# Kernel tuning notes

Measured on AMD Instinct MI355X. Metric: run time of the kernel, lower is better.

## Reference

```python
import jax, jax.numpy as jnp
import numpy as np

B = 128
IN = 256
NLVL = 6
KLVL = 3
CH = 4
C = 4 * CH * CH          # 64 channels per node
OU = 8                   # out_filter_siz_u
OV = 8                   # out_filter_siz_v
NK = 2 ** KLVL           # 8 leaf nodes per axis
W_SCALE = 1.0 / 16.0     # ~1/sqrt(2*2*C) so 7 stacked relu-convs stay numerically sane


def setup_inputs() -> dict:
    key = jax.random.key(0)
    ks = jax.random.split(key, 2 * NLVL + 4)
    fx = IN // 2 ** NLVL  # 4: input patch filter size
    inp = {}
    inp["in_data"] = jax.random.normal(ks[0], (B, IN, IN, 1), jnp.float32)
    inp["in_filter"] = jax.random.normal(ks[1], (fx, fx, 1, C), jnp.float32) * W_SCALE
    inp["in_bias"] = jnp.zeros((C,), jnp.float32)
    i = 2
    for lvl in range(1, NLVL + 1):
        n = 2 ** min(lvl, KLVL)  # node grid: grows to 2^klvl then stays
        inp[f"f{lvl}"] = jax.random.normal(ks[i], (n, n, 2, 2, C, C), jnp.float32) * W_SCALE
        inp[f"b{lvl}"] = jnp.zeros((n, n, C), jnp.float32)
        i += 1
    inp["Wd"] = jax.random.normal(ks[i], (NK, NK, 2, C, OU * OV), jnp.float32) * W_SCALE
    return inp


def _node_conv(x, w, b):
    # x: [Nu,Nv,B,H,W,C]; w: [Nu,Nv,2,2,C,C]; 2x2 stride-2 VALID conv per node
    Nu, Nv, Bn, H, W, Cc = x.shape
    xr = x.reshape(Nu, Nv, Bn, H // 2, 2, W // 2, 2, Cc)
    y = jnp.einsum('uvbhxwyc,uvxyco->uvbhwo', xr, w)
    return jax.nn.relu(y + b[:, :, None, None, None, :])


def _forward(in_data, in_filter, in_bias, fs, bs, Wd):
    Bn = in_data.shape[0]
    fx, fy = in_filter.shape[0], in_filter.shape[1]
    # input interp conv: stride == kernel -> non-overlapping patch GEMM
    xr = in_data[..., 0].reshape(Bn, in_data.shape[1] // fx, fx, in_data.shape[2] // fy, fy)
    x = jax.nn.relu(jnp.einsum('bxpyq,pqc->bxyc', xr, in_filter[:, :, 0, :]) + in_bias)
    x = x[None, None]  # [1,1,B,2^nlvl,2^nlvl,C] node grid
    for lvl in range(1, NLVL + 1):
        if lvl <= KLVL:
            # children (itu,itv) read parent (itu//2, itv//2)
            x = jnp.repeat(jnp.repeat(x, 2, axis=0), 2, axis=1)
        x = _node_conv(x, fs[lvl - 1], bs[lvl - 1])
    feats = x[:, :, :, 0, 0, :]  # [NK,NK,B,C]; spatial is 1x1 at level nlvl
    out = jnp.einsum('uvbc,uvrck->uvbrk', feats, Wd)  # r in {real, imag}
    out = out.reshape(NK, NK, Bn, 2, OU, OV)
    out = jnp.transpose(out, (2, 0, 4, 1, 5, 3))  # [B,itu,ou,itv,ov,2]
    return out.reshape(Bn, NK * OU, NK * OV, 2)


def reference(in_data, in_filter, in_bias, f1, b1, f2, b2, f3, b3, f4, b4, f5, b5, f6, b6, Wd):
    fs = (f1, f2, f3, f4, f5, f6)
    bs = (b1, b2, b3, b4, b5, b6)
    return _forward(in_data, in_filter, in_bias, fs, bs, Wd)
```

## Files before the change

kernel.cpp:

```cpp
#include <hip/hip_runtime.h>
#include <hip/hip_bf16.h>
#include <cstdint>
#include <cstddef>


typedef __attribute__((ext_vector_type(8))) short short8;
typedef __attribute__((ext_vector_type(4))) float f32x4;
typedef unsigned short ushort_t;

static __device__ __forceinline__ float b2f(const __hip_bfloat16 x) {
    return __bfloat162float(x);
}
static __device__ __forceinline__ ushort_t f2bf(float x) {
    __hip_bfloat16 h = __float2bfloat16(x);
    ushort_t u;
    __builtin_memcpy(&u, &h, 2);
    return u;
}
static __device__ __forceinline__ void gl_lds16(const void* g, void* l) {
    __builtin_amdgcn_global_load_lds(
        (const __attribute__((address_space(1))) void*)g,
        (__attribute__((address_space(3))) void*)l, 16, 0, 0);
}
#define WAIT_LGKM0() __builtin_amdgcn_s_waitcnt(0xC07F)
#define WAIT_VM0()   __builtin_amdgcn_s_waitcnt(0x0F70)

#define PREP_BLOCKS 2533

static __device__ __forceinline__ void prep_work(
    int gid, int isbf,
    const void* f1, const void* f2, const void* f3,
    const void* f4, const void* f5, const void* f6, const void* wdsrc,
    const void* b1, const void* b2, const void* b3,
    const void* b4, const void* b5, const void* b6,
    ushort_t* __restrict__ wbuf, ushort_t* __restrict__ wdbuf,
    float* __restrict__ bbuf)
{
    if (gid >= 648448) return;
    if (gid >= 630784) {
        const int bg = gid - 630784;
        const void* src; int base;
        if      (bg <   256) { src = b1; base = 0;     }
        else if (bg <  1280) { src = b2; base = 256;   }
        else if (bg <  5376) { src = b3; base = 1280;  }
        else if (bg <  9472) { src = b4; base = 5376;  }
        else if (bg < 13568) { src = b5; base = 9472;  }
        else                 { src = b6; base = 13568; }
        const int local = bg - base;
        bbuf[bg] = isbf ? b2f(((const __hip_bfloat16*)src)[local])
                        : ((const float*)src)[local];
        return;
    }
    if (gid >= 565248) {
        const int local = gid - 565248;
        const int lane = local & 63;
        const int slot = (local >> 6) & 15;
        const int site = local >> 10;
        const int ks2 = slot >> 3, nh = slot & 7, q = lane >> 4;
        const int n = nh * 16 + (lane & 15);
        const int r = n >> 6, kk = n & 63;
        const int cbase = ks2 * 32 + q * 8;
        ushort_t pk[8];
        if (isbf) {
            const ushort_t* s = (const ushort_t*)wdsrc;
            #pragma unroll
            for (int j = 0; j < 8; j++)
                pk[j] = s[(((size_t)(site * 2 + r) * 64 + cbase + j) * 64) + kk];
        } else {
            const float* s = (const float*)wdsrc;
            #pragma unroll
            for (int j = 0; j < 8; j++)
                pk[j] = f2bf(s[(((size_t)(site * 2 + r) * 64 + cbase + j) * 64) + kk]);
        }
        *(uint4*)&wdbuf[(size_t)local * 8] = *(uint4*)pk;
        return;
    }
    const void* fsrc; int base;
    if      (gid <   8192) { fsrc = f1; base = 0;      }
    else if (gid <  40960) { fsrc = f2; base = 8192;   }
    else if (gid < 172032) { fsrc = f3; base = 40960;  }
    else if (gid < 303104) { fsrc = f4; base = 172032; }
    else if (gid < 434176) { fsrc = f5; base = 303104; }
    else                   { fsrc = f6; base = 434176; }
    const int local = gid - base;
    const int lane = local & 63;
    const int slot = (local >> 6) & 7;
    const int sitetap = local >> 9;
    const int ks = slot >> 2, nh = slot & 3, q = lane >> 4;
    const int n = (lane & 15) + nh * 16;
    const int kbase = ks * 32 + q * 8;
    ushort_t pk[8];
    if (isbf) {
        const ushort_t* s = (const ushort_t*)fsrc + (size_t)sitetap * 4096;
        #pragma unroll
        for (int j = 0; j < 8; j++) pk[j] = s[(kbase + j) * 64 + n];
    } else {
        const float* s = (const float*)fsrc + (size_t)sitetap * 4096;
        #pragma unroll
        for (int j = 0; j < 8; j++) pk[j] = f2bf(s[(kbase + j) * 64 + n]);
    }
    *(uint4*)&wbuf[(size_t)gid * 8] = *(uint4*)pk;
}

static __device__ __forceinline__ void stage0_body(
    int blk, int isbf,
    const void* __restrict__ in_data, const void* __restrict__ filt,
    const void* __restrict__ bias, __hip_bfloat16* __restrict__ x0,
    int b_off, int Bc)
{
    const int X  = blk & 63;
    const int bl = blk >> 6;
    const int bg = bl + b_off;

    __shared__ float sIn[4][256];
    __shared__ float sF[16][64];
    __shared__ float sB[64];

    const int t = threadIdx.x;
    const size_t srow = ((size_t)bg * 256 + (size_t)X * 4) * 256;

    if (isbf) {
        const __hip_bfloat16* src = (const __hip_bfloat16*)in_data + srow;
        #pragma unroll
        for (int i = 0; i < 4; i++) {
            int flat = i * 256 + t;
            int p = flat >> 8, col = flat & 255;
            sIn[p][col] = b2f(src[(size_t)p * 256 + col]);
        }
        const __hip_bfloat16* fsrc = (const __hip_bfloat16*)filt;
        #pragma unroll
        for (int i = 0; i < 4; i++) {
            int flat = i * 256 + t;
            sF[flat >> 6][flat & 63] = b2f(fsrc[flat]);
        }
        if (t < 64) sB[t] = b2f(((const __hip_bfloat16*)bias)[t]);
    } else {
        const float* src = (const float*)in_data + srow;
        const int p = t >> 6, c4 = (t & 63) * 4;
        *(float4*)&sIn[p][c4] = *(const float4*)(src + (size_t)p * 256 + c4);
        const float* fsrc = (const float*)filt;
        #pragma unroll
        for (int i = 0; i < 4; i++) {
            int flat = i * 256 + t;
            sF[flat >> 6][flat & 63] = fsrc[flat];
        }
        if (t < 64) sB[t] = ((const float*)bias)[t];
    }
    __syncthreads();

    const int ty = t >> 4;
    const int tc = t & 15;

    float acc[4][4];
    {
        const float4 bv = *(const float4*)&sB[tc * 4];
        #pragma unroll
        for (int yi = 0; yi < 4; yi++) {
            acc[yi][0] = bv.x; acc[yi][1] = bv.y;
            acc[yi][2] = bv.z; acc[yi][3] = bv.w;
        }
    }

    #pragma unroll
    for (int p = 0; p < 4; p++) {
        float4 rin[4], rf[4];
        #pragma unroll
        for (int yi = 0; yi < 4; yi++)
            rin[yi] = *(const float4*)&sIn[p][ty * 16 + yi * 4];
        #pragma unroll
        for (int q = 0; q < 4; q++)
            rf[q] = *(const float4*)&sF[p * 4 + q][tc * 4];
        #pragma unroll
        for (int yi = 0; yi < 4; yi++) {
            #pragma unroll
            for (int q = 0; q < 4; q++) {
                const float a = ((const float*)&rin[yi])[q];
                acc[yi][0] = fmaf(a, rf[q].x, acc[yi][0]);
                acc[yi][1] = fmaf(a, rf[q].y, acc[yi][1]);
                acc[yi][2] = fmaf(a, rf[q].z, acc[yi][2]);
                acc[yi][3] = fmaf(a, rf[q].w, acc[yi][3]);
            }
        }
    }

    ushort_t* dst = (ushort_t*)x0;
    #pragma unroll
    for (int yi = 0; yi < 4; yi++) {
        uint2 pk;
        pk.x = (uint32_t)f2bf(fmaxf(acc[yi][0], 0.f))
             | ((uint32_t)f2bf(fmaxf(acc[yi][1], 0.f)) << 16);
        pk.y = (uint32_t)f2bf(fmaxf(acc[yi][2], 0.f))
             | ((uint32_t)f2bf(fmaxf(acc[yi][3], 0.f)) << 16);
        const int wpos = ty * 4 + yi;
        *(uint2*)(dst + ((size_t)(X * 64 + wpos) * Bc + bl) * 64 + tc * 4) = pk;
    }
}

__global__ __launch_bounds__(256) void k_prep0(
    const void* __restrict__ in_data,
    const void* f1, const void* f2, const void* f3,
    const void* f4, const void* f5, const void* f6, const void* wdsrc,
    const void* b1, const void* b2, const void* b3,
    const void* b4, const void* b5, const void* b6,
    ushort_t* __restrict__ wbuf, ushort_t* __restrict__ wdbuf,
    float* __restrict__ bbuf, int* __restrict__ flag,
    const void* __restrict__ filt, const void* __restrict__ bias0,
    __hip_bfloat16* __restrict__ x0, int Bc)
{
    __shared__ int sflag;
    const int t = threadIdx.x;
    if (t < 64) {
        const float v = __uint_as_float(((const uint32_t*)in_data)[t]);
        const bool plaus = (v == 0.0f) || (fabsf(v) > 1e-8f && fabsf(v) < 1e4f);
        const unsigned long long m = __ballot(plaus);
        if (t == 0) sflag = (__popcll(m) >= 48) ? 0 : 1;
    }
    __syncthreads();
    const int isbf = sflag;

    if (blockIdx.x < PREP_BLOCKS) {
        if (blockIdx.x == 0 && t == 0) *flag = isbf;
        prep_work(blockIdx.x * 256 + t, isbf,
                  f1, f2, f3, f4, f5, f6, wdsrc,
                  b1, b2, b3, b4, b5, b6, wbuf, wdbuf, bbuf);
    } else {
        stage0_body(blockIdx.x - PREP_BLOCKS, isbf, in_data, filt, bias0, x0, 0, Bc);
    }
}

__global__ __launch_bounds__(256) void k_stage0(
    const void* __restrict__ in_data, const void* __restrict__ filt,
    const void* __restrict__ bias, __hip_bfloat16* __restrict__ x0,
    const int* __restrict__ flag, int b_off, int Bc)
{
    stage0_body(blockIdx.x, *flag, in_data, filt, bias, x0, b_off, Bc);
}

__global__ __launch_bounds__(256, 2) void k_fused12(
    const __hip_bfloat16* __restrict__ xin,
    const ushort_t* __restrict__ w1,
    const ushort_t* __restrict__ w2,
    const float* __restrict__ b1, const float* __restrict__ b2,
    __hip_bfloat16* __restrict__ xout,
    int Bc, int mtiles)
{
    __shared__ __align__(16) ushort_t smem[34816];

    int idx = blockIdx.x;
    const int mt = idx % mtiles; idx /= mtiles;
    const int parent = idx & 3; idx >>= 2;
    const int wstrip = idx & 3;
    const int h2p = idx >> 2;
    const int ip = parent >> 1, jp = parent & 1;

    const int t = threadIdx.x;
    const int wave = t >> 6, lane = t & 63;
    const int lm = lane & 15, lq = lane >> 4;

    const size_t pstride = (size_t)Bc * 64;

    int brow = mt * 16 + lm;
    if (brow >= Bc) brow = Bc - 1;

    const ushort_t* w1site = w1 + (size_t)parent * 16384 + lane * 8;
    short8 breg[32];
    #pragma unroll
    for (int s = 0; s < 32; s++) breg[s] = *(const short8*)(w1site + s * 512);
    __builtin_amdgcn_sched_barrier(0);

    float bv1[4];
    #pragma unroll
    for (int fn = 0; fn < 4; fn++) bv1[fn] = b1[parent * 64 + fn * 16 + lm];

    const f32x4 zero = {0.f, 0.f, 0.f, 0.f};
    ushort_t* l1b = smem + 16384;
    const int wa = wave >> 1, wb = wave & 1;

    for (int pos = 0; pos < 4; pos++) {
        const int w2p = wstrip * 4 + pos;
        __syncthreads();

        #pragma unroll
        for (int k = 0; k < 4; k++) {
            const int lpos = wave * 4 + k;
            const int i0 = lpos >> 2, j0 = lpos & 3;
            const size_t poff =
                ((size_t)(4 * h2p + i0) * 64 + (4 * w2p + j0)) * pstride;
            #pragma unroll
            for (int ks = 0; ks < 2; ks++) {
                gl_lds16(xin + poff + (size_t)brow * 64 + ks * 32 + lq * 8,
                         &smem[(lpos * 2 + ks) * 512]);
            }
        }
        __syncthreads();

        f32x4 acc[4];
        #pragma unroll
        for (int fn = 0; fn < 4; fn++) acc[fn] = zero;
        #pragma unroll
        for (int cd = 0; cd < 4; cd++) {
            const int lpos = (2 * wa + (cd >> 1)) * 4 + (2 * wb + (cd & 1));
            #pragma unroll
            for (int ks = 0; ks < 2; ks++) {
                short8 afr = *(const short8*)&smem[(lpos * 2 + ks) * 512 + lane * 8];
                #pragma unroll
                for (int fn = 0; fn < 4; fn++)
                    acc[fn] = __builtin_amdgcn_mfma_f32_16x16x32_bf16(
                        afr, breg[cd * 8 + ks * 4 + fn], acc[fn], 0, 0, 0);
            }
        }
        ushort_t* dst = l1b + (pos * 4 + wave) * 1152;
        #pragma unroll
        for (int fn = 0; fn < 4; fn++) {
            #pragma unroll
            for (int r = 0; r < 4; r++) {
                const int m = lq * 4 + r;
                dst[m * 72 + fn * 16 + lm] =
                    f2bf(fmaxf(acc[fn][r] + bv1[fn], 0.f));
            }
        }
    }
    __syncthreads();

    {
        const int di = wave >> 1, dj = wave & 1;
        const int s2 = (2 * ip + di) * 4 + (2 * jp + dj);
        const ushort_t* w2site = w2 + (size_t)s2 * 16384 + lane * 8;
        short8 wreg[32];
        #pragma unroll
        for (int s = 0; s < 32; s++) wreg[s] = *(const short8*)(w2site + s * 512);
        __builtin_amdgcn_sched_barrier(0);

        float bv2[4];
        #pragma unroll
        for (int fn = 0; fn < 4; fn++) bv2[fn] = b2[s2 * 64 + fn * 16 + lm];

        ushort_t* so_buf = smem + wave * 2176;

        for (int pos = 0; pos < 4; pos++) {
            const int w2p = wstrip * 4 + pos;
            f32x4 acc[4];
            #pragma unroll
            for (int fn = 0; fn < 4; fn++) acc[fn] = zero;

            #pragma unroll
            for (int ab = 0; ab < 4; ab++) {
                const ushort_t* sl = l1b + (pos * 4 + ab) * 1152;
                #pragma unroll
                for (int ks = 0; ks < 2; ks++) {
                    short8 afr = *(const short8*)&sl[lm * 72 + ks * 32 + lq * 8];
                    #pragma unroll
                    for (int fn = 0; fn < 4; fn++)
                        acc[fn] = __builtin_amdgcn_mfma_f32_16x16x32_bf16(
                            afr, wreg[ab * 8 + ks * 4 + fn], acc[fn], 0, 0, 0);
                }
            }

            #pragma unroll
            for (int fn = 0; fn < 4; fn++) {
                #pragma unroll
                for (int r = 0; r < 4; r++) {
                    const int m = lq * 4 + r;
                    so_buf[m * 68 + fn * 16 + lm] =
                        f2bf(fmaxf(acc[fn][r] + bv2[fn], 0.f));
                }
            }
            const size_t obase = ((size_t)s2 * 256 + h2p * 16 + w2p) * pstride;
            #pragma unroll
            for (int i2 = 0; i2 < 2; i2++) {
                const int task = i2 * 64 + lane;
                const int oct = task & 7, row = task >> 3;
                const int brw = mt * 16 + row;
                if (brw < Bc) {
                    *(uint4*)(xout + obase + (size_t)brw * 64 + oct * 8) =
                        *(const uint4*)&so_buf[row * 68 + oct * 8];
                }
            }
        }
    }
}

__global__ __launch_bounds__(256, 2) void k_level4(
    const __hip_bfloat16* __restrict__ xin,
    const ushort_t* __restrict__ wbuf,
    const float* __restrict__ bbuf,
    __hip_bfloat16* __restrict__ xout,
    int Nv_out, int HW, int Bc, int mtiles)
{
    __shared__ __align__(16) ushort_t smem[17408];

    int idx = blockIdx.x;
    const int mt = idx % mtiles; idx /= mtiles;
    const int w  = idx % HW; idx /= HW;
    const int h  = idx % HW; idx /= HW;
    const int Nv_in = Nv_out >> 1;
    const int vp = idx % Nv_in;
    const int up = idx / Nv_in;

    const int t = threadIdx.x;
    const int wave = t >> 6, lane = t & 63;
    const int lm = lane & 15, lq = lane >> 4;

    const int so = (2 * up + (wave >> 1)) * Nv_out + (2 * vp + (wave & 1));
    const int H_in = HW * 2;
    const size_t pstride = (size_t)Bc * 64;
    const size_t siteb = (size_t)(up * Nv_in + vp) * H_in * H_in * pstride;
    const ushort_t* wsite = wbuf + (size_t)so * 4 * 4096 + lane * 8;

    {
        const int hi = 2 * h + (wave >> 1), wi = 2 * w + (wave & 1);
        const size_t tapoff = siteb + ((size_t)hi * H_in + wi) * pstride;
        #pragma unroll
        for (int j = 0; j < 8; j++) {
            const int ks = j >> 2, mh = j & 3;
            int b = mt * 64 + mh * 16 + lm;
            if (b >= Bc) b = Bc - 1;
            gl_lds16(xin + tapoff + (size_t)b * 64 + ks * 32 + lq * 8,
                     &smem[(wave * 8 + j) * 512]);
        }
    }

    short8 breg[32];
    #pragma unroll
    for (int s = 0; s < 32; s++)
        breg[s] = *(const short8*)(wsite + s * 512);
    __builtin_amdgcn_sched_barrier(0);

    float bv[4];
    #pragma unroll
    for (int fn = 0; fn < 4; fn++) bv[fn] = bbuf[so * 64 + fn * 16 + lm];

    __syncthreads();

    const f32x4 zero = {0.f, 0.f, 0.f, 0.f};
    f32x4 acc[4][4];
    #pragma unroll
    for (int i = 0; i < 4; i++)
        #pragma unroll
        for (int j = 0; j < 4; j++) acc[i][j] = zero;

    #pragma unroll
    for (int tap = 0; tap < 4; tap++) {
        #pragma unroll
        for (int ks = 0; ks < 2; ks++) {
            #pragma unroll
            for (int fm = 0; fm < 4; fm++) {
                short8 a = *(const short8*)&smem[(tap * 8 + ks * 4 + fm) * 512 + lane * 8];
                #pragma unroll
                for (int fn = 0; fn < 4; fn++)
                    acc[fm][fn] = __builtin_amdgcn_mfma_f32_16x16x32_bf16(
                        a, breg[tap * 8 + ks * 4 + fn], acc[fm][fn], 0, 0, 0);
            }
        }
    }
    __syncthreads();

    ushort_t* so_buf = smem + wave * 4352;
    #pragma unroll
    for (int fm = 0; fm < 4; fm++) {
        #pragma unroll
        for (int fn = 0; fn < 4; fn++) {
            #pragma unroll
            for (int r = 0; r < 4; r++) {
                const int row = fm * 16 + lq * 4 + r;
                so_buf[row * 68 + fn * 16 + lm] =
                    f2bf(fmaxf(acc[fm][fn][r] + bv[fn], 0.f));
            }
        }
    }
    __syncthreads();

    const size_t obase = ((size_t)so * HW * HW + (size_t)h * HW + w) * pstride;
    #pragma unroll
    for (int i = 0; i < 8; i++) {
        const int task = i * 64 + lane;
        const int oct = task & 7, row = task >> 3;
        const int b = mt * 64 + row;
        if (b < Bc) {
            *(uint4*)(xout + obase + (size_t)b * 64 + oct * 8) =
                *(const uint4*)&so_buf[row * 68 + oct * 8];
        }
    }
}

__global__ __launch_bounds__(256) void k_f456(
    const __hip_bfloat16* __restrict__ xin,
    const ushort_t* __restrict__ w4, const ushort_t* __restrict__ w5,
    const ushort_t* __restrict__ w6, const ushort_t* __restrict__ wd,
    const float* __restrict__ b4, const float* __restrict__ b5,
    const float* __restrict__ b6,
    void* __restrict__ out, const int* __restrict__ flag,
    int Bc, int b_off, int mtiles)
{
    const int isbf = *flag;
    const int bx = blockIdx.x;
    const int mt = bx % mtiles;
    const int site = bx / mtiles;
    const int u = site >> 3, v = site & 7;

    __shared__ __align__(16) ushort_t smem[37376];

    const int t = threadIdx.x;
    const int wv = t >> 6, lane = t & 63;
    const int lm = lane & 15, lq = lane >> 4;

    const ushort_t* w6s = w6 + (size_t)site * 16384 + lane * 8;
    const ushort_t* wds = wd + (size_t)site * 8192  + lane * 8;

    float bv4[4], bv5[4];
    #pragma unroll
    for (int fn = 0; fn < 4; fn++) {
        bv4[fn] = b4[site * 64 + fn * 16 + lm];
        bv5[fn] = b5[site * 64 + fn * 16 + lm];
    }
    const float bv6 = b6[site * 64 + wv * 16 + lm];

    {
        const ushort_t* w4s = w4 + (size_t)site * 16384;
        #pragma unroll
        for (int s2 = 0; s2 < 8; s2++) {
            const int s = wv * 8 + s2;
            gl_lds16(w4s + s * 512 + lane * 8, &smem[s * 512]);
        }
    }
    __syncthreads();

    const f32x4 zero = {0.f, 0.f, 0.f, 0.f};
    const int h5 = wv >> 1, w5p = wv & 1;
    ushort_t* mid1w = smem + 16384 + wv * 4224;
    ushort_t* Aw = smem + 33280 + wv * 1024;
    const size_t pstride = (size_t)Bc * 64;

    int brow = mt * 16 + lm;
    if (brow >= Bc) brow = Bc - 1;
    const __hip_bfloat16* xbase =
        xin + (size_t)site * 64 * pstride + (size_t)brow * 64 + lq * 8;

    for (int i = 0; i < 4; i++) {
        const int h4 = 2 * h5 + (i >> 1), w4p = 2 * w5p + (i & 1);
        f32x4 acc[4];
        #pragma unroll
        for (int b_ = 0; b_ < 4; b_++) acc[b_] = zero;

        for (int tap = 0; tap < 4; tap++) {
            const int h3 = 2 * h4 + (tap >> 1), w3 = 2 * w4p + (tap & 1);
            const size_t poff = (size_t)(h3 * 8 + w3) * pstride;
            WAIT_LGKM0();
            #pragma unroll
            for (int ks = 0; ks < 2; ks++) {
                gl_lds16(xbase + poff + ks * 32, &Aw[ks * 512]);
            }
            WAIT_VM0();
            __builtin_amdgcn_sched_barrier(0);
            #pragma unroll
            for (int ks = 0; ks < 2; ks++) {
                short8 a = *(const short8*)&Aw[ks * 512 + lane * 8];
                #pragma unroll
                for (int fn = 0; fn < 4; fn++) {
                    short8 bfr = *(const short8*)&smem[(tap * 8 + ks * 4 + fn) * 512 + lane * 8];
                    acc[fn] = __builtin_amdgcn_mfma_f32_16x16x32_bf16(a, bfr, acc[fn], 0, 0, 0);
                }
            }
        }
        #pragma unroll
        for (int fn = 0; fn < 4; fn++) {
            #pragma unroll
            for (int r = 0; r < 4; r++) {
                const int m = lq * 4 + r;
                const int ch = fn * 16 + lm;
                mid1w[m * 264 + i * 64 + ch] =
                    f2bf(fmaxf(acc[fn][r] + bv4[fn], 0.f));
            }
        }
    }
    __syncthreads();

    {
        const ushort_t* w5s = w5 + (size_t)site * 16384;
        #pragma unroll
        for (int s2 = 0; s2 < 8; s2++) {
            const int s = wv * 8 + s2;
            gl_lds16(w5s + s * 512 + lane * 8, &smem[s * 512]);
        }
    }
    __syncthreads();

    short8 b3r[8];
    short8 wdr[4];
    {
        f32x4 acc2[4];
        #pragma unroll
        for (int b_ = 0; b_ < 4; b_++) acc2[b_] = zero;

        #pragma unroll
        for (int i = 0; i < 4; i++) {
            #pragma unroll
            for (int ks = 0; ks < 2; ks++) {
                short8 a0 = *(const short8*)&mid1w[lm * 264 + i * 64 + ks * 32 + lq * 8];
                #pragma unroll
                for (int fn = 0; fn < 4; fn++) {
                    short8 bfr = *(const short8*)&smem[(i * 8 + ks * 4 + fn) * 512 + lane * 8];
                    acc2[fn] = __builtin_amdgcn_mfma_f32_16x16x32_bf16(a0, bfr, acc2[fn], 0, 0, 0);
                }
            }
        }

        #pragma unroll
        for (int tap = 0; tap < 4; tap++)
            #pragma unroll
            for (int ks = 0; ks < 2; ks++)
                b3r[tap * 2 + ks] = *(const short8*)(w6s + (tap * 8 + ks * 4 + wv) * 512);
        #pragma unroll
        for (int ks = 0; ks < 2; ks++)
            #pragma unroll
            for (int n2 = 0; n2 < 2; n2++)
                wdr[ks * 2 + n2] = *(const short8*)(wds + (ks * 8 + 2 * wv + n2) * 512);

        #pragma unroll
        for (int fn = 0; fn < 4; fn++) {
            #pragma unroll
            for (int r = 0; r < 4; r++) {
                const int m = lq * 4 + r;
                const int ch = fn * 16 + lm;
                mid1w[m * 72 + ch] =
                    f2bf(fmaxf(acc2[fn][r] + bv5[fn], 0.f));
            }
        }
    }
    __syncthreads();

    {
        f32x4 acc3 = zero;
        #pragma unroll
        for (int tap = 0; tap < 4; tap++) {
            const ushort_t* sl = smem + 16384 + tap * 4224;
            #pragma unroll
            for (int ks = 0; ks < 2; ks++) {
                short8 a0 = *(const short8*)&sl[lm * 72 + ks * 32 + lq * 8];
                acc3 = __builtin_amdgcn_mfma_f32_16x16x32_bf16(a0, b3r[tap * 2 + ks], acc3, 0, 0, 0);
            }
        }
        ushort_t* mid3 = smem + 33280;
        #pragma unroll
        for (int r = 0; r < 4; r++) {
            const int m = lq * 4 + r;
            const int ch = wv * 16 + lm;
            mid3[m * 72 + ch] = f2bf(fmaxf(acc3[r] + bv6, 0.f));
        }
    }
    __syncthreads();

    {
        const ushort_t* mid3 = smem + 33280;
        f32x4 acc4[2];
        acc4[0] = zero; acc4[1] = zero;
        #pragma unroll
        for (int ks = 0; ks < 2; ks++) {
            short8 a0 = *(const short8*)&mid3[lm * 72 + ks * 32 + lq * 8];
            #pragma unroll
            for (int n2 = 0; n2 < 2; n2++) {
                acc4[n2] = __builtin_amdgcn_mfma_f32_16x16x32_bf16(a0, wdr[ks * 2 + n2], acc4[n2], 0, 0, 0);
            }
        }
        #pragma unroll
        for (int n2 = 0; n2 < 2; n2++) {
            const int n = (2 * wv + n2) * 16 + lm;
            const int rr = n >> 6, ou = (n >> 3) & 7, ov = n & 7;
            const size_t obase =
                (((size_t)(u * 8 + ou)) * 64 + (v * 8 + ov)) * 2 + rr;
            #pragma unroll
            for (int reg = 0; reg < 4; reg++) {
                const int brw = mt * 16 + lq * 4 + reg;
                if (brw < Bc) {
                    const size_t oidx = obase + (size_t)(b_off + brw) * 8192;
                    if (isbf) ((__hip_bfloat16*)out)[oidx] =
                        __float2bfloat16(acc4[n2][reg]);
                    else ((float*)out)[oidx] = acc4[n2][reg];
                }
            }
        }
    }
}

extern "C" void kernel_launch(void* const* d_in, const int* in_sizes, int n_in,
                              void* d_out, int out_size, void* d_ws, size_t ws_size,
                              hipStream_t stream)
{
    (void)in_sizes; (void)n_in; (void)out_size;

    const void* in_data = d_in[0];
    const void* filt    = d_in[1];
    const void* bias0   = d_in[2];
    const void* fl[7];
    const void* bl[7];
    for (int l = 1; l <= 6; l++) {
        fl[l] = d_in[1 + 2 * l];
        bl[l] = d_in[2 + 2 * l];
    }
    const void* Wd = d_in[15];

    const int Bfull = 128;
    const size_t perB = (size_t)64 * 64 * 64;

    const size_t wbufBytes  = 565248ull * 16;
    const size_t wdbufBytes = 65536ull * 16;
    const size_t bbufBytes  = 17664ull * 4;
    const size_t headBytes  = 256 + wbufBytes + wdbufBytes + bbufBytes;

    const size_t avail = ws_size > headBytes ? ws_size - headBytes : 0;
    int Bc = 0;
    for (int c = 128; c >= 1; c >>= 1) {
        if ((size_t)2 * c * perB * sizeof(__hip_bfloat16) <= avail) { Bc = c; break; }
    }
    if (Bc == 0) return;

    int* flag = (int*)d_ws;
    ushort_t* wbuf  = (ushort_t*)((char*)d_ws + 256);
    ushort_t* wdbuf = (ushort_t*)((char*)d_ws + 256 + wbufBytes);
    float* bbuf = (float*)((char*)d_ws + 256 + wbufBytes + wdbufBytes);
    __hip_bfloat16* bufA = (__hip_bfloat16*)((char*)d_ws + headBytes);
    __hip_bfloat16* bufB = bufA + (size_t)Bc * perB;

    const int mt4  = (Bc + 63) / 64;
    const int mt16 = (Bc + 15) / 16;

    for (int b_off = 0; b_off < Bfull; b_off += Bc) {
        if (b_off == 0) {
            k_prep0<<<dim3(PREP_BLOCKS + Bc * 64), 256, 0, stream>>>(
                in_data,
                fl[1], fl[2], fl[3], fl[4], fl[5], fl[6], Wd,
                bl[1], bl[2], bl[3], bl[4], bl[5], bl[6],
                wbuf, wdbuf, bbuf, flag,
                filt, bias0, bufA, Bc);
        } else {
            k_stage0<<<dim3(Bc * 64), 256, 0, stream>>>(in_data, filt, bias0, bufA, flag, b_off, Bc);
        }

        k_fused12<<<dim3(256 * mt16), 256, 0, stream>>>(
            bufA, wbuf, wbuf + 65536, bbuf, bbuf + 256, bufB, Bc, mt16);

        {
            dim3 grid(4 * 4 * 8 * 8 * mt4);
            k_level4<<<grid, 256, 0, stream>>>(bufB, wbuf + 327680,
                bbuf + 1280, bufA, 8, 8, Bc, mt4);
        }

        k_f456<<<dim3(64 * mt16), 256, 0, stream>>>(bufA,
            wbuf + 1376256, wbuf + 2424832, wbuf + 3473408, wdbuf,
            bbuf + 5376, bbuf + 9472, bbuf + 13568,
            d_out, flag, Bc, b_off, mt16);
    }
}
```

Before: 243.0 us.

## Load level-1 A fragments directly from global and store outputs without LDS staging

In the fused level-1/2 kernel, the input tiles are no longer staged through LDS with global_load_lds and barriers. Each wave now reads its A fragments straight from global memory. The level-2 output also skips the LDS transpose buffer and writes scalar bf16 values directly to global. Together these shrink shared memory to the intermediate buffer only, allowing the launch bound to rise from 2 to 4 blocks per CU. The trade-off is uncoalesced 2-byte global stores, redundant global reads across waves, and more register pressure under the tighter occupancy bound, which may cause spills with 32 weight fragments held per thread.

```diff
diff --git a/kernel.cpp b/kernel.cpp
--- a/kernel.cpp
+++ b/kernel.cpp
@@ -236,7 +236,7 @@
     stage0_body(blockIdx.x, *flag, in_data, filt, bias, x0, b_off, Bc);
 }
 
-__global__ __launch_bounds__(256, 2) void k_fused12(
+__global__ __launch_bounds__(256, 4) void k_fused12(
     const __hip_bfloat16* __restrict__ xin,
     const ushort_t* __restrict__ w1,
     const ushort_t* __restrict__ w2,
@@ -244,7 +244,7 @@
     __hip_bfloat16* __restrict__ xout,
     int Bc, int mtiles)
 {
-    __shared__ __align__(16) ushort_t smem[34816];
+    __shared__ __align__(16) ushort_t l1b[18432];
 
     int idx = blockIdx.x;
     const int mt = idx % mtiles; idx /= mtiles;
@@ -266,43 +266,30 @@
     short8 breg[32];
     #pragma unroll
     for (int s = 0; s < 32; s++) breg[s] = *(const short8*)(w1site + s * 512);
-    __builtin_amdgcn_sched_barrier(0);
 
     float bv1[4];
     #pragma unroll
     for (int fn = 0; fn < 4; fn++) bv1[fn] = b1[parent * 64 + fn * 16 + lm];
 
     const f32x4 zero = {0.f, 0.f, 0.f, 0.f};
-    ushort_t* l1b = smem + 16384;
     const int wa = wave >> 1, wb = wave & 1;
 
     for (int pos = 0; pos < 4; pos++) {
         const int w2p = wstrip * 4 + pos;
-        __syncthreads();
-
-        #pragma unroll
-        for (int k = 0; k < 4; k++) {
-            const int lpos = wave * 4 + k;
-            const int i0 = lpos >> 2, j0 = lpos & 3;
-            const size_t poff =
-                ((size_t)(4 * h2p + i0) * 64 + (4 * w2p + j0)) * pstride;
+        f32x4 acc[4];
+        #pragma unroll
+        for (int fn = 0; fn < 4; fn++) acc[fn] = zero;
+
+        #pragma unroll
+        for (int cd = 0; cd < 4; cd++) {
+            const int hi0 = 4 * h2p + 2 * wa + (cd >> 1);
+            const int wi0 = 4 * w2p + 2 * wb + (cd & 1);
+            const __hip_bfloat16* ap =
+                xin + ((size_t)hi0 * 64 + wi0) * pstride
+                    + (size_t)brow * 64 + lq * 8;
             #pragma unroll
             for (int ks = 0; ks < 2; ks++) {
-                gl_lds16(xin + poff + (size_t)brow * 64 + ks * 32 + lq * 8,
-                         &smem[(lpos * 2 + ks) * 512]);
-            }
-        }
-        __syncthreads();
-
-        f32x4 acc[4];
-        #pragma unroll
-        for (int fn = 0; fn < 4; fn++) acc[fn] = zero;
-        #pragma unroll
-        for (int cd = 0; cd < 4; cd++) {
-            const int lpos = (2 * wa + (cd >> 1)) * 4 + (2 * wb + (cd & 1));
-            #pragma unroll
-            for (int ks = 0; ks < 2; ks++) {
-                short8 afr = *(const short8*)&smem[(lpos * 2 + ks) * 512 + lane * 8];
+                short8 afr = *(const short8*)(ap + ks * 32);
                 #pragma unroll
                 for (int fn = 0; fn < 4; fn++)
                     acc[fn] = __builtin_amdgcn_mfma_f32_16x16x32_bf16(
@@ -329,13 +316,12 @@
         short8 wreg[32];
         #pragma unroll
         for (int s = 0; s < 32; s++) wreg[s] = *(const short8*)(w2site + s * 512);
-        __builtin_amdgcn_sched_barrier(0);
 
         float bv2[4];
         #pragma unroll
         for (int fn = 0; fn < 4; fn++) bv2[fn] = b2[s2 * 64 + fn * 16 + lm];
 
-        ushort_t* so_buf = smem + wave * 2176;
+        ushort_t* outp = (ushort_t*)xout;
 
         for (int pos = 0; pos < 4; pos++) {
             const int w2p = wstrip * 4 + pos;
@@ -356,24 +342,17 @@
                 }
             }
 
+            const size_t obase = ((size_t)s2 * 256 + h2p * 16 + w2p) * pstride;
             #pragma unroll
             for (int fn = 0; fn < 4; fn++) {
                 #pragma unroll
                 for (int r = 0; r < 4; r++) {
                     const int m = lq * 4 + r;
-                    so_buf[m * 68 + fn * 16 + lm] =
-                        f2bf(fmaxf(acc[fn][r] + bv2[fn], 0.f));
-                }
-            }
-            const size_t obase = ((size_t)s2 * 256 + h2p * 16 + w2p) * pstride;
-            #pragma unroll
-            for (int i2 = 0; i2 < 2; i2++) {
-                const int task = i2 * 64 + lane;
-                const int oct = task & 7, row = task >> 3;
-                const int brw = mt * 16 + row;
-                if (brw < Bc) {
-                    *(uint4*)(xout + obase + (size_t)brw * 64 + oct * 8) =
-                        *(const uint4*)&so_buf[row * 68 + oct * 8];
+                    const int brw = mt * 16 + m;
+                    if (brw < Bc) {
+                        outp[obase + (size_t)brw * 64 + fn * 16 + lm] =
+                            f2bf(fmaxf(acc[fn][r] + bv2[fn], 0.f));
+                    }
                 }
             }
         }
```

Measured after the change: 332.4 us. +36.8%, slower.
